# Kernel optimization log

Measured on AMD Instinct MI355X. Metric: run time of the kernel, lower is better.

## Reference

```python
import jax, jax.numpy as jnp
import numpy as np

N, E, G = 8000, 128000, 4
C, NLM, NL = 64, 16, 4
NEL, NB, NH = 10, 8, 64
RMAX = 5.0
PCUT = 5.0
AVG_NEIGH = 16.0
SIGMA = 1.0
LBOX = 6.0
KR = 3
T = 2
LMAP = jnp.array([0, 1, 1, 1, 2, 2, 2, 2, 2, 3, 3, 3, 3, 3, 3, 3])


def _nvec():
    r = np.arange(-KR, KR + 1)
    n = np.stack(np.meshgrid(r, r, r, indexing='ij'), -1).reshape(-1, 3)
    n = n[np.any(n != 0, axis=1)]  # [342,3], k=0 excluded
    return jnp.asarray(n, jnp.float32)


def sph_harm(u):
    # component-normalized real spherical harmonics up to l=3, unit input u [E,3]
    x, y, z = u[:, 0], u[:, 1], u[:, 2]
    one = jnp.ones_like(x)
    c3, c5, c15 = 3.0 ** 0.5, 5.0 ** 0.5, 15.0 ** 0.5
    Y = [one,
         c3 * x, c3 * y, c3 * z,
         c15 * x * y, c15 * y * z, 0.5 * c5 * (3 * z * z - 1.0), c15 * x * z, 0.5 * c15 * (x * x - y * y),
         (35.0 / 8.0) ** 0.5 * y * (3 * x * x - y * y), 105.0 ** 0.5 * x * y * z,
         (21.0 / 8.0) ** 0.5 * y * (5 * z * z - 1.0), 0.5 * 7.0 ** 0.5 * z * (5 * z * z - 3.0),
         (21.0 / 8.0) ** 0.5 * x * (5 * z * z - 1.0), 0.5 * 105.0 ** 0.5 * z * (x * x - y * y),
         (35.0 / 8.0) ** 0.5 * x * (x * x - 3 * y * y)]
    return jnp.stack(Y, -1)  # [E,16]


def radial_basis(r):
    # Bessel basis * polynomial cutoff (MACE RadialEmbeddingBlock)
    u = r / RMAX
    n = jnp.arange(1, NB + 1, dtype=jnp.float32)
    bes = (2.0 / RMAX) ** 0.5 * jnp.sin(n[None, :] * jnp.pi * u[:, None]) / (r[:, None] + 1e-9)
    p = PCUT
    fc = 1.0 - 0.5 * (p + 1) * (p + 2) * u ** p + p * (p + 2) * u ** (p + 1) - 0.5 * p * (p + 1) * u ** (p + 2)
    fc = fc * (u < 1.0)
    return bes * fc[:, None]  # [E,8]


def setup_inputs() -> dict:
    key = jax.random.key(0)
    ks = jax.random.split(key, 24)

    def p(k, shape, fan_in):
        return jax.random.normal(k, shape, jnp.float32) / (fan_in ** 0.5)

    elem = jax.random.randint(ks[0], (N,), 0, NEL)
    inp = {
        'node_attrs': jax.nn.one_hot(elem, NEL, dtype=jnp.float32),
        'positions': jax.random.uniform(ks[1], (N, 3), jnp.float32) * LBOX,
        'shifts': jnp.zeros((E, 3), jnp.float32),
        'density_coefficients': jax.random.normal(ks[2], (N, 1), jnp.float32) * 0.1,
        'cell': jnp.tile(jnp.eye(3, dtype=jnp.float32) * LBOX, (G, 1, 1)),
        'rcell': jnp.tile(jnp.eye(3, dtype=jnp.float32) / LBOX, (G, 1, 1)),
        'volume': jnp.full((G,), LBOX ** 3, jnp.float32),
        'edge_index': jax.random.randint(ks[3], (2, E), 0, N),
        'batch': jnp.repeat(jnp.arange(G), N // G),
        'emb_W': p(ks[4], (NEL, C), NEL),
        'q_coef': p(ks[5], (T, C), 1),
        'rad_W1': p(ks[6], (T, NB, NH), NB),
        'rad_W2': p(ks[7], (T, NH, NH), NH),
        'rad_W3': p(ks[8], (T, NH, NH), NH),
        'rad_W4': p(ks[9], (T, NH, C * NL), NH),
        'lin_up': p(ks[10], (T, NL, C, C), C),
        'lin_out': p(ks[11], (T, NL, C, C), C),
        'W_sc': p(ks[12], (T, NEL, C, C), C),
        'Wp': p(ks[13], (T, 3, C, C), C),
        'W_read0': p(ks[14], (C,), C),
        'Wread1_a': p(ks[15], (C, 16), C),
        'Wread1_b': p(ks[16], (16,), 16),
        'Wq_read': p(ks[17], (T, C), C),
        'atomic_E': jax.random.normal(ks[18], (NEL,), jnp.float32),
    }
    return inp


def reference(node_attrs, positions, shifts, density_coefficients, cell, rcell, volume,
              edge_index, batch, emb_W, q_coef, rad_W1, rad_W2, rad_W3, rad_W4,
              lin_up, lin_out, W_sc, Wp, W_read0, Wread1_a, Wread1_b, Wq_read, atomic_E):
    sender, receiver = edge_index[0], edge_index[1]
    vec = positions[receiver] - positions[sender] + shifts
    r = jnp.linalg.norm(vec, axis=-1)
    Y = sph_harm(vec / (r[:, None] + 1e-9))      # [E,16]
    ef = radial_basis(r)                          # [E,8]

    q = density_coefficients                      # [N,1], max_l=0 multipoles
    feats = jnp.zeros((N, C, NLM), jnp.float32).at[:, :, 0].set(node_attrs @ emb_W)
    e0 = jax.ops.segment_sum(node_attrs @ atomic_E, batch, G)
    energies = [e0]

    for t in range(T):
        # charge-coefficient injection (charge_coefs_linears)
        feats = feats.at[:, :, 0].add(q * q_coef[t][None, :])
        # per-l linear up
        h = jnp.einsum('ncl,lcd->ndl', feats, lin_up[t][LMAP])
        # radial MLP -> per-edge, per-channel, per-l tensor-product weights
        w = jax.nn.silu(ef @ rad_W1[t])
        w = jax.nn.silu(w @ rad_W2[t])
        w = jax.nn.silu(w @ rad_W3[t])
        w = (w @ rad_W4[t]).reshape(E, C, NL)[:, :, LMAP]   # [E,C,16]
        # depthwise equivariant TP message: gather -> contract -> modulate
        hj = h[sender]                                       # [E,C,16]
        s_e = jnp.einsum('ecl,el->ec', hj, Y)                # edge invariant
        m = w * (Y[:, None, :] * s_e[:, :, None])            # [E,C,16]
        A = jax.ops.segment_sum(m, receiver, N) / AVG_NEIGH  # scatter-reduce
        A = jnp.einsum('ncl,lcd->ndl', A, lin_out[t][LMAP])
        # element-dependent residual (self-connection)
        wn = jnp.einsum('nk,kcd->ncd', node_attrs, W_sc[t])
        sc = jnp.einsum('ncd,ncl->ndl', wn, feats)
        # product block: correlation-3 symmetric-contraction surrogate
        s1 = jnp.sum(A * A, axis=2)                           # [N,C]
        out = (jnp.einsum('ncl,cd->ndl', A, Wp[t, 0])
               + jnp.einsum('ncl,cd->ndl', A * s1[:, :, None], Wp[t, 1])
               + jnp.einsum('ncl,cd->ndl', A * (s1 * s1)[:, :, None], Wp[t, 2]))
        feats = out + sc
        # readout
        if t == T - 1:
            node_e = jax.nn.silu(feats[:, :, 0] @ Wread1_a) @ Wread1_b
        else:
            node_e = feats[:, :, 0] @ W_read0
        node_e = node_e + q[:, 0] * (feats[:, :, 0] @ Wq_read[t])
        energies.append(jax.ops.segment_sum(node_e, batch, G))

    # k-space (Ewald-like) electrostatics with Gaussian-smeared charges
    nv = _nvec()                                              # [K,3]
    kvec = 2.0 * jnp.pi * jnp.einsum('kj,gji->gki', nv, rcell)  # [G,K,3]
    k2 = jnp.sum(kvec * kvec, -1)                             # [G,K]
    phase = jnp.einsum('ni,nki->nk', positions, kvec[batch])  # [N,K]
    Sr = jax.ops.segment_sum(q * jnp.cos(phase), batch, G)
    Si = jax.ops.segment_sum(q * jnp.sin(phase), batch, G)
    filt = jnp.exp(-0.5 * SIGMA * SIGMA * k2) / k2
    Ees = (2.0 * jnp.pi / volume) * jnp.sum(filt * (Sr * Sr + Si * Si), axis=1)

    total_energy = jnp.sum(jnp.stack(energies, -1), -1) + Ees
    total_charge = jax.ops.segment_sum(q[:, 0], batch, G)
    dipole = jax.ops.segment_sum(q * positions, batch, G)
    return total_energy, total_charge, dipole
```

## Files before the change

### kernel.cpp

```cpp
#include <hip/hip_runtime.h>
#include <hip/hip_bf16.h>

constexpr int N    = 8000;
constexpr int E    = 128000;
constexpr int G    = 4;
constexpr int NEL  = 10;
constexpr int NGR  = N / G;
constexpr int NC   = N * 64;
constexpr int NK   = 342;
constexpr float RMAX = 5.0f;
constexpr int HS = 72;
constexpr int WS2 = 260;
constexpr int WT_T = 25088;

typedef __bf16 bf16x8 __attribute__((ext_vector_type(8)));
typedef float  f32x4v __attribute__((ext_vector_type(4)));
typedef unsigned short u16x8 __attribute__((ext_vector_type(8)));

__device__ __forceinline__ int lmap_rt(int l) { return (l >= 1) + (l >= 4) + (l >= 9); }
__device__ __forceinline__ float silu(float x) { return x / (1.f + __expf(-x)); }
__device__ __forceinline__ float bf2f(unsigned short u) { return __uint_as_float(((unsigned)u) << 16); }
__device__ __forceinline__ unsigned short f2bf(float f) {
    __hip_bfloat16 h = __float2bfloat16(f);
    return *(unsigned short*)&h;
}

__device__ __forceinline__ void mfma_stage(const unsigned short* hsrc, const unsigned short* wt,
                                           int m0, int lane, f32x4v acc[4], bool k8only)
{
    const int quad = lane >> 4;
    const int idx  = lane & 15;
    bf16x8 bz;
    #pragma unroll
    for (int i = 0; i < 8; ++i) bz[i] = (__bf16)0.f;
    bf16x8 a0 = bz, a1 = bz;
    const int mrow = m0 + idx;
    if (k8only) {
        if (quad == 0) a0 = *(const bf16x8*)&hsrc[mrow * HS];
    } else {
        a0 = *(const bf16x8*)&hsrc[mrow * HS + (quad << 3)];
        a1 = *(const bf16x8*)&hsrc[mrow * HS + 32 + (quad << 3)];
    }
    #pragma unroll
    for (int c4 = 0; c4 < 4; ++c4) {
        const int nrow = (c4 << 4) + idx;
        if (k8only) {
            bf16x8 b0 = bz;
            if (quad == 0) b0 = *(const bf16x8*)&wt[nrow * HS];
            acc[c4] = __builtin_amdgcn_mfma_f32_16x16x32_bf16(a0, b0, acc[c4], 0, 0, 0);
        } else {
            const bf16x8 b0 = *(const bf16x8*)&wt[nrow * HS + (quad << 3)];
            const bf16x8 b1 = *(const bf16x8*)&wt[nrow * HS + 32 + (quad << 3)];
            acc[c4] = __builtin_amdgcn_mfma_f32_16x16x32_bf16(a0, b0, acc[c4], 0, 0, 0);
            acc[c4] = __builtin_amdgcn_mfma_f32_16x16x32_bf16(a1, b1, acc[c4], 0, 0, 0);
        }
    }
}

__global__ __launch_bounds__(256) void k_init(const float* __restrict__ na,
    const float* __restrict__ q, const float* __restrict__ pos,
    const int* __restrict__ batch, const float* __restrict__ aE,
    int* __restrict__ elem, int* __restrict__ counts, float* __restrict__ acc)
{
    __shared__ float s[G * 5];
    if (threadIdx.x < G * 5) s[threadIdx.x] = 0.f;
    __syncthreads();
    const int n = blockIdx.x * 256 + threadIdx.x;
    if (n < N) {
        int el = 0; float best = na[n * NEL];
        #pragma unroll
        for (int j = 1; j < NEL; ++j) { float v = na[n * NEL + j]; if (v > best) { best = v; el = j; } }
        elem[n] = el;
        atomicAdd(&counts[el], 1);
        const int g = batch[n];
        const float qn = q[n];
        atomicAdd(&s[g * 5 + 0], aE[el]);
        atomicAdd(&s[g * 5 + 1], qn);
        atomicAdd(&s[g * 5 + 2], qn * pos[n * 3 + 0]);
        atomicAdd(&s[g * 5 + 3], qn * pos[n * 3 + 1]);
        atomicAdd(&s[g * 5 + 4], qn * pos[n * 3 + 2]);
    }
    __syncthreads();
    if (threadIdx.x < G * 5) atomicAdd(&acc[threadIdx.x], s[threadIdx.x]);
}

__global__ __launch_bounds__(256) void k_feat0(const int* __restrict__ elem,
    const float* __restrict__ embW, float* __restrict__ F)
{
    const int i = blockIdx.x * 256 + threadIdx.x;
    if (i < NC) F[i] = embW[elem[i >> 6] * 64 + (i & 63)];
}

__global__ void k_offs(const int* __restrict__ counts, int* __restrict__ offs)
{
    if (threadIdx.x == 0 && blockIdx.x == 0) {
        int o = 0;
        for (int j = 0; j < NEL; ++j) { offs[j] = o; o += (counts[j] + 63) & ~63; }
        offs[NEL] = o;
    }
}
__global__ __launch_bounds__(256) void k_scatter(const int* __restrict__ elem,
    const int* __restrict__ offs, int* __restrict__ cursor, int* __restrict__ perm)
{
    const int n = blockIdx.x * 256 + threadIdx.x;
    if (n < N) {
        const int el = elem[n];
        const int p = atomicAdd(&cursor[el], 1);
        perm[offs[el] + p] = n;
    }
}

__global__ __launch_bounds__(256) void k_gcnt(const int* __restrict__ ei, int* __restrict__ cnt)
{
    const int e = blockIdx.x * 256 + threadIdx.x;
    if (e < E) atomicAdd(&cnt[ei[E + e]], 1);
}
__global__ __launch_bounds__(1024) void k_goff(const int* __restrict__ cnt, int* __restrict__ roff)
{
    __shared__ int part[1024];
    const int t = threadIdx.x;
    const int base = t * 8;
    int loc[8];
    int s = 0;
    #pragma unroll
    for (int i = 0; i < 8; ++i) { loc[i] = s; s += (base + i < N) ? cnt[base + i] : 0; }
    part[t] = s;
    __syncthreads();
    for (int d = 1; d < 1024; d <<= 1) {
        const int v = (t >= d) ? part[t - d] : 0;
        __syncthreads();
        part[t] += v;
        __syncthreads();
    }
    const int excl = (t == 0) ? 0 : part[t - 1];
    #pragma unroll
    for (int i = 0; i < 8; ++i) if (base + i < N) roff[base + i] = excl + loc[i];
    if (t == 0) roff[N] = E;
}
__global__ __launch_bounds__(256) void k_gscat(const int* __restrict__ ei,
    const int* __restrict__ roff, int* __restrict__ cur, int* __restrict__ elist)
{
    const int e = blockIdx.x * 256 + threadIdx.x;
    if (e < E) {
        const int rv = ei[E + e];
        const int p = atomicAdd(&cur[rv], 1);
        elist[roff[rv] + p] = e;
    }
}

__global__ __launch_bounds__(256) void k_geom(const float* __restrict__ pos,
    const float* __restrict__ shifts, const int* __restrict__ ei,
    const int* __restrict__ elist, float4* __restrict__ geomv, int* __restrict__ spck)
{
    const int j = blockIdx.x * 256 + threadIdx.x;
    if (j >= E) return;
    const int e = elist[j];
    const int s = ei[e], rv = ei[E + e];
    const float dx = pos[rv * 3 + 0] - pos[s * 3 + 0] + shifts[e * 3 + 0];
    const float dy = pos[rv * 3 + 1] - pos[s * 3 + 1] + shifts[e * 3 + 1];
    const float dz = pos[rv * 3 + 2] - pos[s * 3 + 2] + shifts[e * 3 + 2];
    const float r = sqrtf(dx * dx + dy * dy + dz * dz);
    const float inv = 1.f / (r + 1e-9f);
    float4 g;
    g.x = dx * inv; g.y = dy * inv; g.z = dz * inv; g.w = r;
    geomv[j] = g;
    spck[j] = s;
}

__global__ __launch_bounds__(256) void k_wprep_all(const float* __restrict__ rW1,
    const float* __restrict__ rW2, const float* __restrict__ rW3,
    const float* __restrict__ rW4, const float* __restrict__ Wp,
    const float* __restrict__ lup, const float* __restrict__ lout,
    const float* __restrict__ Wsc,
    unsigned short* __restrict__ WT, unsigned short* __restrict__ WpT,
    unsigned short* __restrict__ WlupT, unsigned short* __restrict__ WloutT,
    unsigned short* __restrict__ WscT)
{
    const int gidx = blockIdx.x * 256 + threadIdx.x;
    if (gidx < 2 * WT_T) {
        const int t = gidx / WT_T;
        const int r = gidx % WT_T;
        float v;
        if (r < 512) {
            const int n = r >> 3, k = r & 7;
            v = rW1[t * 512 + k * 64 + n];
        } else if (r < 4608) {
            const int i = r - 512, n = i >> 6, k = i & 63;
            v = rW2[t * 4096 + k * 64 + n];
        } else if (r < 8704) {
            const int i = r - 4608, n = i >> 6, k = i & 63;
            v = rW3[t * 4096 + k * 64 + n];
        } else {
            const int i = r - 8704, n = i >> 6, k = i & 63;
            v = rW4[t * 16384 + k * 256 + n];
        }
        WT[gidx] = f2bf(v);
    } else if (gidx < 2 * WT_T + 24576) {
        const int idx = gidx - 2 * WT_T;
        const int i  = idx & 4095;
        const int d = i >> 6, c = i & 63;
        WpT[idx] = f2bf(Wp[(size_t)(idx >> 12) * 4096 + c * 64 + d]);
    } else if (gidx < 2 * WT_T + 24576 + 32768) {
        const int idx = gidx - (2 * WT_T + 24576);
        const int i = idx & 4095, d = i >> 6, c = i & 63;
        WlupT[idx] = f2bf(lup[(idx >> 12) * 4096 + c * 64 + d]);
    } else if (gidx < 2 * WT_T + 24576 + 65536) {
        const int idx = gidx - (2 * WT_T + 24576 + 32768);
        const int i = idx & 4095, d = i >> 6, c = i & 63;
        WloutT[idx] = f2bf(lout[(idx >> 12) * 4096 + c * 64 + d]);
    } else if (gidx < 2 * WT_T + 24576 + 65536 + 81920) {
        const int idx = gidx - (2 * WT_T + 24576 + 65536);
        const int i = idx & 4095, d = i >> 6, c = i & 63;
        WscT[idx] = f2bf(Wsc[(idx >> 12) * 4096 + c * 64 + d]);
    }
}

__global__ __launch_bounds__(256) void k_lgemm_hb(float* __restrict__ F,
    const float* __restrict__ q, const float* __restrict__ qc,
    const unsigned short* __restrict__ WT, unsigned short* __restrict__ Hb)
{
    __shared__ unsigned short Xb[64 * HS];
    __shared__ unsigned short Wt[64 * HS];
    const int l  = blockIdx.y;
    const int nb = blockIdx.x << 6;
    const int t  = threadIdx.x;
    const int lane = t & 63;
    const int m0   = (t >> 6) << 4;
    const int quad = lane >> 4;
    const int idx  = lane & 15;
    const int prow = t >> 2, pkb = (t & 3) << 4;
    float* Xp = F + (size_t)l * NC + (size_t)nb * 64;
    if (l == 0) {
        #pragma unroll
        for (int k = 0; k < 16; ++k) {
            const int i = t + (k << 8);
            float v = Xp[i] + q[nb + (i >> 6)] * qc[i & 63];
            Xp[i] = v;
            Xb[(i >> 6) * HS + (i & 63)] = f2bf(v);
        }
    } else {
        #pragma unroll
        for (int k = 0; k < 16; ++k) {
            const int i = t + (k << 8);
            Xb[(i >> 6) * HS + (i & 63)] = f2bf(Xp[i]);
        }
    }
    const unsigned short* W = WT + lmap_rt(l) * 4096;
    *(u16x8*)&Wt[prow * HS + pkb]     = *(const u16x8*)&W[prow * 64 + pkb];
    *(u16x8*)&Wt[prow * HS + pkb + 8] = *(const u16x8*)&W[prow * 64 + pkb + 8];
    __syncthreads();
    f32x4v acc[4];
    #pragma unroll
    for (int c = 0; c < 4; ++c) { acc[c][0] = 0.f; acc[c][1] = 0.f; acc[c][2] = 0.f; acc[c][3] = 0.f; }
    mfma_stage(Xb, Wt, m0, lane, acc, false);
    #pragma unroll
    for (int c4 = 0; c4 < 4; ++c4) {
        #pragma unroll
        for (int r = 0; r < 4; ++r) {
            const int n = nb + m0 + (quad << 2) + r;
            const int col = (c4 << 4) + idx;
            Hb[(size_t)n * 1024 + (l << 6) + col] = f2bf(acc[c4][r]);
        }
    }
}

__global__ __launch_bounds__(256) void k_hbT(const unsigned short* __restrict__ Hb,
    unsigned short* __restrict__ HbT)
{
    const int n = (blockIdx.x << 2) + (threadIdx.x >> 6);
    const int c = threadIdx.x & 63;
    u16x8 a, b;
    #pragma unroll
    for (int l = 0; l < 8; ++l) {
        a[l] = Hb[(size_t)n * 1024 + (l << 6) + c];
        b[l] = Hb[(size_t)n * 1024 + ((l + 8) << 6) + c];
    }
    *(u16x8*)&HbT[(size_t)n * 1024 + c * 16]     = a;
    *(u16x8*)&HbT[(size_t)n * 1024 + c * 16 + 8] = b;
}

__global__ __launch_bounds__(256) void k_lgemm(const float* __restrict__ X,
    const unsigned short* __restrict__ WT, float* __restrict__ Out)
{
    __shared__ unsigned short Xb[64 * HS];
    __shared__ unsigned short Wt[64 * HS];
    const int l  = blockIdx.y;
    const int nb = blockIdx.x << 6;
    const int t  = threadIdx.x;
    const int lane = t & 63;
    const int m0   = (t >> 6) << 4;
    const int quad = lane >> 4;
    const int idx  = lane & 15;
    const int prow = t >> 2, pkb = (t & 3) << 4;
    const float* Xp = X + (size_t)l * NC + (size_t)nb * 64;
    #pragma unroll
    for (int k = 0; k < 16; ++k) {
        const int i = t + (k << 8);
        Xb[(i >> 6) * HS + (i & 63)] = f2bf(Xp[i]);
    }
    const unsigned short* W = WT + lmap_rt(l) * 4096;
    *(u16x8*)&Wt[prow * HS + pkb]     = *(const u16x8*)&W[prow * 64 + pkb];
    *(u16x8*)&Wt[prow * HS + pkb + 8] = *(const u16x8*)&W[prow * 64 + pkb + 8];
    __syncthreads();
    f32x4v acc[4];
    #pragma unroll
    for (int c = 0; c < 4; ++c) { acc[c][0] = 0.f; acc[c][1] = 0.f; acc[c][2] = 0.f; acc[c][3] = 0.f; }
    mfma_stage(Xb, Wt, m0, lane, acc, false);
    float* Op = Out + (size_t)l * NC + (size_t)nb * 64;
    #pragma unroll
    for (int c4 = 0; c4 < 4; ++c4) {
        #pragma unroll
        for (int r = 0; r < 4; ++r) {
            const int row = m0 + (quad << 2) + r;
            Op[(row << 6) + (c4 << 4) + idx] = acc[c4][r];
        }
    }
}

__global__ __launch_bounds__(256) void k_sc(const float* __restrict__ F,
    const unsigned short* __restrict__ WscT, const int* __restrict__ perm,
    const int* __restrict__ elem, float* __restrict__ Out)
{
    __shared__ unsigned short Xb[64 * HS];
    __shared__ unsigned short Wt[64 * HS];
    __shared__ int rows[64];
    const int l  = blockIdx.y;
    const int tb = blockIdx.x << 6;
    const int t  = threadIdx.x;
    if (t < 64) rows[t] = perm[tb + t];
    __syncthreads();
    if (rows[0] < 0) return;
    const int lane = t & 63;
    const int m0   = (t >> 6) << 4;
    const int quad = lane >> 4;
    const int idx  = lane & 15;
    const int prow = t >> 2, pkb = (t & 3) << 4;
    const unsigned short* W = WscT + elem[rows[0]] * 4096;
    *(u16x8*)&Wt[prow * HS + pkb]     = *(const u16x8*)&W[prow * 64 + pkb];
    *(u16x8*)&Wt[prow * HS + pkb + 8] = *(const u16x8*)&W[prow * 64 + pkb + 8];
    #pragma unroll
    for (int k = 0; k < 16; ++k) {
        const int i = t + (k << 8);
        const int rr = i >> 6, cc = i & 63;
        const int n = rows[rr];
        Xb[rr * HS + cc] = (n >= 0) ? f2bf(F[(size_t)l * NC + (size_t)n * 64 + cc]) : (unsigned short)0;
    }
    __syncthreads();
    f32x4v acc[4];
    #pragma unroll
    for (int c = 0; c < 4; ++c) { acc[c][0] = 0.f; acc[c][1] = 0.f; acc[c][2] = 0.f; acc[c][3] = 0.f; }
    mfma_stage(Xb, Wt, m0, lane, acc, false);
    #pragma unroll
    for (int c4 = 0; c4 < 4; ++c4) {
        #pragma unroll
        for (int r = 0; r < 4; ++r) {
            const int n = rows[m0 + (quad << 2) + r];
            if (n >= 0) Out[(size_t)l * NC + (size_t)n * 64 + (c4 << 4) + idx] = acc[c4][r];
        }
    }
}

__global__ __launch_bounds__(256) void k_edge(const float4* __restrict__ geomv,
    const int* __restrict__ spck, const unsigned short* __restrict__ WT,
    const unsigned short* __restrict__ HbT, const int* __restrict__ roff,
    float* __restrict__ A)
{
    __shared__ unsigned short hbf[64 * HS];
    __shared__ unsigned short wtb[64 * HS];
    __shared__ unsigned short wfull[64 * WS2];
    __shared__ float geos[64 * 4];
    __shared__ int   sps[64];
    __shared__ int   rinfo[2];
    const int t = threadIdx.x;
    const int lane = t & 63;
    const int wid  = t >> 6;
    const int m0   = wid << 4;
    const int quad = lane >> 4;
    const int idx  = lane & 15;
    const int prow = t >> 2, pkb = (t & 3) << 4;
    const int w0 = blockIdx.x << 6;
    const int w1 = w0 + 64;
    if (t == 0) {
        int lo = 0, hi = N - 1;
        while (lo < hi) { const int mid = (lo + hi + 1) >> 1; if (roff[mid] <= w0) lo = mid; else hi = mid - 1; }
        rinfo[0] = lo;
    } else if (t == 1) {
        const int w1m = w0 + 63;
        int lo = 0, hi = N - 1;
        while (lo < hi) { const int mid = (lo + hi + 1) >> 1; if (roff[mid] <= w1m) lo = mid; else hi = mid - 1; }
        rinfo[1] = lo;
    }
    if (t < 64) {
        const float4 g = geomv[w0 + t];
        *(float4*)&geos[t * 4] = g;
        sps[t] = spck[w0 + t];
        const float r = g.w;
        const float u  = r * 0.2f;
        const float u2 = u * u, u5 = u2 * u2 * u;
        const float fc = 1.f - 21.f * u5 + 35.f * u5 * u - 15.f * u5 * u2;
        float pref = 0.63245553f * fc / (r + 1e-9f);
        if (u >= 1.f) pref = 0.f;
        const float piu = 3.14159265358979f * u;
        #pragma unroll
        for (int b = 0; b < 8; ++b) hbf[t * HS + b] = f2bf(__sinf((float)(b + 1) * piu) * pref);
    }
    {
        const int n = t >> 2, k = (t & 3) << 1;
        wtb[n * HS + k]     = WT[n * 8 + k];
        wtb[n * HS + k + 1] = WT[n * 8 + k + 1];
    }
    u16x8 pf0 = *(const u16x8*)&WT[512 + prow * 64 + pkb];
    u16x8 pf1 = *(const u16x8*)&WT[512 + prow * 64 + pkb + 8];
    __syncthreads();
    f32x4v acc[4];
    #pragma unroll
    for (int c = 0; c < 4; ++c) { acc[c][0] = 0.f; acc[c][1] = 0.f; acc[c][2] = 0.f; acc[c][3] = 0.f; }
    mfma_stage(hbf, wtb, m0, lane, acc, true);
    __syncthreads();
    #pragma unroll
    for (int c4 = 0; c4 < 4; ++c4)
        #pragma unroll
        for (int r = 0; r < 4; ++r)
            hbf[(m0 + (quad << 2) + r) * HS + (c4 << 4) + idx] = f2bf(silu(acc[c4][r]));
    *(u16x8*)&wtb[prow * HS + pkb]     = pf0;
    *(u16x8*)&wtb[prow * HS + pkb + 8] = pf1;
    pf0 = *(const u16x8*)&WT[4608 + prow * 64 + pkb];
    pf1 = *(const u16x8*)&WT[4608 + prow * 64 + pkb + 8];
    __syncthreads();
    #pragma unroll
    for (int c = 0; c < 4; ++c) { acc[c][0] = 0.f; acc[c][1] = 0.f; acc[c][2] = 0.f; acc[c][3] = 0.f; }
    mfma_stage(hbf, wtb, m0, lane, acc, false);
    __syncthreads();
    #pragma unroll
    for (int c4 = 0; c4 < 4; ++c4)
        #pragma unroll
        for (int r = 0; r < 4; ++r)
            hbf[(m0 + (quad << 2) + r) * HS + (c4 << 4) + idx] = f2bf(silu(acc[c4][r]));
    *(u16x8*)&wtb[prow * HS + pkb]     = pf0;
    *(u16x8*)&wtb[prow * HS + pkb + 8] = pf1;
    pf0 = *(const u16x8*)&WT[8704 + prow * 64 + pkb];
    pf1 = *(const u16x8*)&WT[8704 + prow * 64 + pkb + 8];
    __syncthreads();
    #pragma unroll
    for (int c = 0; c < 4; ++c) { acc[c][0] = 0.f; acc[c][1] = 0.f; acc[c][2] = 0.f; acc[c][3] = 0.f; }
    mfma_stage(hbf, wtb, m0, lane, acc, false);
    __syncthreads();
    #pragma unroll
    for (int c4 = 0; c4 < 4; ++c4)
        #pragma unroll
        for (int r = 0; r < 4; ++r)
            hbf[(m0 + (quad << 2) + r) * HS + (c4 << 4) + idx] = f2bf(silu(acc[c4][r]));
    *(u16x8*)&wtb[prow * HS + pkb]     = pf0;
    *(u16x8*)&wtb[prow * HS + pkb + 8] = pf1;
    pf0 = *(const u16x8*)&WT[8704 + 4096 + prow * 64 + pkb];
    pf1 = *(const u16x8*)&WT[8704 + 4096 + prow * 64 + pkb + 8];
    __syncthreads();
    for (int cc = 0; cc < 4; ++cc) {
        #pragma unroll
        for (int c = 0; c < 4; ++c) { acc[c][0] = 0.f; acc[c][1] = 0.f; acc[c][2] = 0.f; acc[c][3] = 0.f; }
        mfma_stage(hbf, wtb, m0, lane, acc, false);
        __syncthreads();
        #pragma unroll
        for (int c4 = 0; c4 < 4; ++c4)
            #pragma unroll
            for (int r = 0; r < 4; ++r)
                wfull[(m0 + (quad << 2) + r) * WS2 + (cc << 6) + (c4 << 4) + idx] = f2bf(acc[c4][r]);
        if (cc < 3) {
            *(u16x8*)&wtb[prow * HS + pkb]     = pf0;
            *(u16x8*)&wtb[prow * HS + pkb + 8] = pf1;
            if (cc < 2) {
                pf0 = *(const u16x8*)&WT[8704 + (cc + 2) * 4096 + prow * 64 + pkb];
                pf1 = *(const u16x8*)&WT[8704 + (cc + 2) * 4096 + prow * 64 + pkb + 8];
            }
        }
        __syncthreads();
    }
    const int r0 = rinfo[0], r1 = rinfo[1];
    constexpr int LM[16] = {0,1,1,1,2,2,2,2,2,3,3,3,3,3,3,3};
    for (int r = r0 + wid; r <= r1; r += 4) {
        const int ra = roff[r], rb = roff[r + 1];
        const int ja = ra > w0 ? ra : w0;
        const int jb = rb < w1 ? rb : w1;
        float a16[16];
        #pragma unroll
        for (int l = 0; l < 16; ++l) a16[l] = 0.f;
        if (ja < jb) {
            u16x8 hA0, hB0, hA1, hB1;
            {
                const int s = sps[ja - w0];
                hA0 = *(const u16x8*)&HbT[(size_t)s * 1024 + lane * 16];
                hB0 = *(const u16x8*)&HbT[(size_t)s * 1024 + lane * 16 + 8];
            }
            hA1 = hA0; hB1 = hB0;
            if (ja + 1 < jb) {
                const int s = sps[ja + 1 - w0];
                hA1 = *(const u16x8*)&HbT[(size_t)s * 1024 + lane * 16];
                hB1 = *(const u16x8*)&HbT[(size_t)s * 1024 + lane * 16 + 8];
            }
            for (int j = ja; j < jb; ++j) {
                const int jj = j - w0;
                float hc[16];
                #pragma unroll
                for (int l = 0; l < 8; ++l) { hc[l] = bf2f(hA0[l]); hc[l + 8] = bf2f(hB0[l]); }
                hA0 = hA1; hB0 = hB1;
                if (j + 2 < jb) {
                    const int s = sps[jj + 2];
                    hA1 = *(const u16x8*)&HbT[(size_t)s * 1024 + lane * 16];
                    hB1 = *(const u16x8*)&HbT[(size_t)s * 1024 + lane * 16 + 8];
                }
                const float gr = geos[jj * 4 + 3];
                if (gr >= RMAX) continue;
                const float x = geos[jj * 4], y = geos[jj * 4 + 1], z = geos[jj * 4 + 2];
                const float xx = x * x, yy = y * y, zz = z * z;
                float Y[16];
                Y[0] = 1.f;
                Y[1] = 1.7320508f * x;  Y[2] = 1.7320508f * y;  Y[3] = 1.7320508f * z;
                Y[4] = 3.8729833f * x * y;  Y[5] = 3.8729833f * y * z;
                Y[6] = 0.5f * 2.2360680f * (3.f * zz - 1.f);
                Y[7] = 3.8729833f * x * z;  Y[8] = 0.5f * 3.8729833f * (xx - yy);
                Y[9]  = 2.0916500f * y * (3.f * xx - yy);
                Y[10] = 10.2469508f * x * y * z;
                Y[11] = 1.6201852f * y * (5.f * zz - 1.f);
                Y[12] = 0.5f * 2.6457513f * z * (5.f * zz - 3.f);
                Y[13] = 1.6201852f * x * (5.f * zz - 1.f);
                Y[14] = 0.5f * 10.2469508f * z * (xx - yy);
                Y[15] = 2.0916500f * x * (xx - 3.f * yy);
                float se = 0.f;
                #pragma unroll
                for (int l = 0; l < 16; ++l) se += hc[l] * Y[l];
                se *= 0.0625f;
                const ushort4 wq = *(const ushort4*)&wfull[jj * WS2 + (lane << 2)];
                const float wl[4] = { bf2f(wq.x) * se, bf2f(wq.y) * se, bf2f(wq.z) * se, bf2f(wq.w) * se };
                #pragma unroll
                for (int l = 0; l < 16; ++l) a16[l] += wl[LM[l]] * Y[l];
            }
        }
        float* Ap = A + (size_t)r * 64 + lane;
        if (ra >= w0 && rb <= w1) {
            #pragma unroll
            for (int l = 0; l < 16; ++l) Ap[(size_t)l * NC] = a16[l];
        } else {
            #pragma unroll
            for (int l = 0; l < 16; ++l) atomicAdd(&Ap[(size_t)l * NC], a16[l]);
        }
    }
}

__global__ __launch_bounds__(256) void k_s1(const float* __restrict__ H, float* __restrict__ s1)
{
    const int i = blockIdx.x * 256 + threadIdx.x;
    if (i < NC) {
        float s = 0.f;
        #pragma unroll
        for (int l = 0; l < 16; ++l) { const float a = H[(size_t)l * NC + i]; s += a * a; }
        s1[i] = s;
    }
}

__global__ __launch_bounds__(256) void k_out(const float* __restrict__ Ap,
    const float* __restrict__ s1, const unsigned short* __restrict__ WpT,
    const float* __restrict__ sc, float* __restrict__ F)
{
    __shared__ unsigned short Xb[64 * HS];
    __shared__ unsigned short Wt[64 * HS];
    const int l  = blockIdx.y;
    const int nb = blockIdx.x << 6;
    const int t  = threadIdx.x;
    const int lane = t & 63;
    const int m0   = (t >> 6) << 4;
    const int quad = lane >> 4;
    const int idx  = lane & 15;
    const int prow = t >> 2, pkb = (t & 3) << 4;
    const float* Xp = Ap + (size_t)l * NC + (size_t)nb * 64;
    float av[16], sv[16];
    #pragma unroll
    for (int k = 0; k < 16; ++k) {
        const int i = t + (k << 8);
        av[k] = Xp[i];
        sv[k] = s1[nb * 64 + i];
    }
    f32x4v acc[4];
    #pragma unroll
    for (int c = 0; c < 4; ++c) { acc[c][0] = 0.f; acc[c][1] = 0.f; acc[c][2] = 0.f; acc[c][3] = 0.f; }
    for (int p = 0; p < 3; ++p) {
        #pragma unroll
        for (int k = 0; k < 16; ++k) {
            const int i = t + (k << 8);
            Xb[(i >> 6) * HS + (i & 63)] = f2bf(av[k]);
            av[k] *= sv[k];
        }
        *(u16x8*)&Wt[prow * HS + pkb]     = *(const u16x8*)&WpT[p * 4096 + prow * 64 + pkb];
        *(u16x8*)&Wt[prow * HS + pkb + 8] = *(const u16x8*)&WpT[p * 4096 + prow * 64 + pkb + 8];
        __syncthreads();
        mfma_stage(Xb, Wt, m0, lane, acc, false);
        __syncthreads();
    }
    #pragma unroll
    for (int c4 = 0; c4 < 4; ++c4) {
        #pragma unroll
        for (int r = 0; r < 4; ++r) {
            const int row = m0 + (quad << 2) + r;
            const int col = (c4 << 4) + idx;
            const size_t id = (size_t)l * NC + (size_t)(nb + row) * 64 + col;
            F[id] = acc[c4][r] + sc[id];
        }
    }
}

__global__ __launch_bounds__(256) void k_read(const float* __restrict__ F,
    const float* __restrict__ q, const int* __restrict__ batch,
    const float* __restrict__ Wr0, const float* __restrict__ Wa,
    const float* __restrict__ Wb, const float* __restrict__ Wq,
    float* __restrict__ acc, int last)
{
    __shared__ float sred[G];
    if (threadIdx.x < G) sred[threadIdx.x] = 0.f;
    __syncthreads();
    const int n = blockIdx.x * 256 + threadIdx.x;
    if (n < N) {
        float a16[16];
        #pragma unroll
        for (int j = 0; j < 16; ++j) a16[j] = 0.f;
        float ar = 0.f, aq = 0.f;
        const float* f = F + (size_t)n * 64;
        for (int c = 0; c < 64; ++c) {
            const float fv = f[c];
            aq += fv * Wq[c];
            if (last) {
                #pragma unroll
                for (int j = 0; j < 16; ++j) a16[j] += fv * Wa[c * 16 + j];
            } else ar += fv * Wr0[c];
        }
        float en;
        if (last) {
            en = 0.f;
            #pragma unroll
            for (int j = 0; j < 16; ++j) en += silu(a16[j]) * Wb[j];
        } else en = ar;
        en += q[n] * aq;
        atomicAdd(&sred[batch[n]], en);
    }
    __syncthreads();
    if (threadIdx.x < G) atomicAdd(&acc[threadIdx.x * 5], sred[threadIdx.x]);
}

__global__ __launch_bounds__(256) void k_kvec(const float* __restrict__ rcell,
    float* __restrict__ kvec, float* __restrict__ k2)
{
    const int idx = blockIdx.x * 256 + threadIdx.x;
    if (idx >= G * NK) return;
    const int g = idx / NK, k = idx % NK;
    const int kk = k + (k >= 171 ? 1 : 0);
    const int a = kk / 49 - 3, b = (kk / 7) % 7 - 3, c = kk % 7 - 3;
    const float* rc = rcell + g * 9;
    float s = 0.f;
    #pragma unroll
    for (int i = 0; i < 3; ++i) {
        const float kv = 6.283185307f * ((float)a * rc[0 + i] + (float)b * rc[3 + i] + (float)c * rc[6 + i]);
        kvec[idx * 3 + i] = kv;
        s += kv * kv;
    }
    k2[idx] = s;
}

__global__ __launch_bounds__(256) void k_phase(const float* __restrict__ pos,
    const float* __restrict__ q, const float* __restrict__ kvec,
    float* __restrict__ Sr, float* __restrict__ Si)
{
    __shared__ float kvs[38 * 3];
    __shared__ float srs[38], sis[38];
    const int g = blockIdx.z, kc = blockIdx.x, ncb = blockIdx.y;
    const int kbase = kc * 38;
    if (threadIdx.x < 38 * 3) kvs[threadIdx.x] = kvec[((size_t)g * NK + kbase) * 3 + threadIdx.x];
    if (threadIdx.x < 38) { srs[threadIdx.x] = 0.f; sis[threadIdx.x] = 0.f; }
    __syncthreads();
    const int t = threadIdx.x;
    float px = 0.f, py = 0.f, pz = 0.f, qn = 0.f;
    if (t < 250) {
        const int n = g * NGR + ncb * 250 + t;
        px = pos[n * 3]; py = pos[n * 3 + 1]; pz = pos[n * 3 + 2]; qn = q[n];
    }
    const int lane = t & 63;
    for (int j = 0; j < 38; ++j) {
        const float ph = px * kvs[j * 3] + py * kvs[j * 3 + 1] + pz * kvs[j * 3 + 2];
        float sv, cv;
        __sincosf(ph, &sv, &cv);
        float vr = qn * cv, vi = qn * sv;
        #pragma unroll
        for (int o = 32; o > 0; o >>= 1) { vr += __shfl_down(vr, o, 64); vi += __shfl_down(vi, o, 64); }
        if (lane == 0) { atomicAdd(&srs[j], vr); atomicAdd(&sis[j], vi); }
    }
    __syncthreads();
    if (t < 38) {
        atomicAdd(&Sr[g * NK + kbase + t], srs[t]);
        atomicAdd(&Si[g * NK + kbase + t], sis[t]);
    }
}

__global__ __launch_bounds__(512) void k_final(const float* __restrict__ k2,
    const float* __restrict__ Sr, const float* __restrict__ Si,
    const float* __restrict__ vol, const float* __restrict__ acc,
    float* __restrict__ out)
{
    __shared__ float red[512];
    const int g = blockIdx.x, t = threadIdx.x;
    float v = 0.f;
    if (t < NK) {
        const float kk = k2[g * NK + t];
        const float sr = Sr[g * NK + t], si = Si[g * NK + t];
        v = __expf(-0.5f * kk) * (sr * sr + si * si) / kk;
    }
    red[t] = v;
    __syncthreads();
    for (int s2 = 256; s2 > 0; s2 >>= 1) {
        if (t < s2) red[t] += red[t + s2];
        __syncthreads();
    }
    if (t == 0) {
        const float Ees = 6.283185307f / vol[g] * red[0];
        out[g]     = acc[g * 5 + 0] + Ees;
        out[4 + g] = acc[g * 5 + 1];
        out[8 + g * 3 + 0] = acc[g * 5 + 2];
        out[8 + g * 3 + 1] = acc[g * 5 + 3];
        out[8 + g * 3 + 2] = acc[g * 5 + 4];
    }
}

extern "C" void kernel_launch(void* const* d_in, const int* in_sizes, int n_in,
                              void* d_out, int out_size, void* d_ws, size_t ws_size,
                              hipStream_t stream)
{
    const float* na    = (const float*)d_in[0];
    const float* pos   = (const float*)d_in[1];
    const float* shif  = (const float*)d_in[2];
    const float* q     = (const float*)d_in[3];
    const float* rcell = (const float*)d_in[5];
    const float* vol   = (const float*)d_in[6];
    const int*   ei    = (const int*)d_in[7];
    const int*   batch = (const int*)d_in[8];
    const float* embW  = (const float*)d_in[9];
    const float* qcoef = (const float*)d_in[10];
    const float* rW1   = (const float*)d_in[11];
    const float* rW2   = (const float*)d_in[12];
    const float* rW3   = (const float*)d_in[13];
    const float* rW4   = (const float*)d_in[14];
    const float* lup   = (const float*)d_in[15];
    const float* lout  = (const float*)d_in[16];
    const float* Wsc   = (const float*)d_in[17];
    const float* Wp    = (const float*)d_in[18];
    const float* Wr0   = (const float*)d_in[19];
    const float* Wa    = (const float*)d_in[20];
    const float* Wb    = (const float*)d_in[21];
    const float* Wq    = (const float*)d_in[22];
    const float* aE    = (const float*)d_in[23];
    float* out = (float*)d_out;

    float* wsf  = (float*)d_ws;
    float* F    = wsf;
    float* A    = F + 8192000;
    float* R    = A + 8192000;
    float* H2   = R;
    unsigned short* HbT   = (unsigned short*)R;
    unsigned short* Hbtmp = (unsigned short*)(R + 4096000);
    float* s1   = R + 20480000;
    float* kvec = s1 + 512000;
    float* k2   = kvec + 4104;
    float* Sr   = k2 + 1368;
    float* Si   = Sr + 1368;
    float* acc  = Si + 1368;
    int*   elem = (int*)(acc + 32);
    int*   perm = elem + 8000;
    int*   counts = perm + 8640;
    int*   cursor = counts + 16;
    int*   offs   = cursor + 16;
    int*   roff   = offs + 16;
    int*   cnt    = roff + 8001;
    int*   cur    = cnt + 8000;
    int*   elist  = cur + 8000;
    unsigned short* WTb = (unsigned short*)(((uintptr_t)(elist + E) + 31) & ~(uintptr_t)31);
    unsigned short* WpT = WTb + 2 * WT_T;
    float4* geomv = (float4*)(WpT + 24576);
    int*    spck  = (int*)(geomv + E);
    unsigned short* WlupT  = (unsigned short*)(spck + E);
    unsigned short* WloutT = WlupT + 32768;
    unsigned short* WscT   = WloutT + 32768;

    hipMemsetAsync(F, 0, 8192000 * sizeof(float), stream);
    hipMemsetAsync(Sr, 0, (1368 * 2 + 32) * sizeof(float), stream);
    hipMemsetAsync(perm, 0xFF, 8640 * sizeof(int), stream);
    hipMemsetAsync(counts, 0, 32 * sizeof(int), stream);
    hipMemsetAsync(cnt, 0, 16000 * sizeof(int), stream);

    k_init<<<32, 256, 0, stream>>>(na, q, pos, batch, aE, elem, counts, acc);
    k_feat0<<<2000, 256, 0, stream>>>(elem, embW, F);
    k_offs<<<1, 64, 0, stream>>>(counts, offs);
    k_scatter<<<32, 256, 0, stream>>>(elem, offs, cursor, perm);
    k_gcnt<<<500, 256, 0, stream>>>(ei, cnt);
    k_goff<<<1, 1024, 0, stream>>>(cnt, roff);
    k_gscat<<<500, 256, 0, stream>>>(ei, roff, cur, elist);
    k_geom<<<500, 256, 0, stream>>>(pos, shif, ei, elist, geomv, spck);
    k_wprep_all<<<868, 256, 0, stream>>>(rW1, rW2, rW3, rW4, Wp, lup, lout, Wsc,
                                         WTb, WpT, WlupT, WloutT, WscT);
    k_kvec<<<6, 256, 0, stream>>>(rcell, kvec, k2);
    k_phase<<<dim3(9, 8, G), 256, 0, stream>>>(pos, q, kvec, Sr, Si);

    for (int t = 0; t < 2; ++t) {
        k_lgemm_hb<<<dim3(125, 16), 256, 0, stream>>>(F, q, qcoef + t * 64, WlupT + t * 16384, Hbtmp);
        k_hbT<<<2000, 256, 0, stream>>>(Hbtmp, HbT);
        hipMemsetAsync(A, 0, 8192000 * sizeof(float), stream);
        k_edge<<<2000, 256, 0, stream>>>(geomv, spck, WTb + t * WT_T, HbT, roff, A);
        k_lgemm<<<dim3(125, 16), 256, 0, stream>>>(A, WloutT + t * 16384, H2);
        k_s1<<<2000, 256, 0, stream>>>(H2, s1);
        k_sc<<<dim3(135, 16), 256, 0, stream>>>(F, WscT + t * 40960, perm, elem, A);
        k_out<<<dim3(125, 16), 256, 0, stream>>>(H2, s1, WpT + t * 12288, A, F);
        k_read<<<32, 256, 0, stream>>>(F, q, batch, Wr0, Wa, Wb, Wq + t * 64, acc, t == 1);
    }
    k_final<<<G, 512, 0, stream>>>(k2, Sr, Si, vol, acc, out);
}
```

Before: 564.3 us.

## Store node features, H2 and self-connection buffers in bf16 with vectorized loads

Node feature tensor F, the linear-out result H2 and the self-connection output are now stored as bf16 instead of fp32. This halves the memory traffic across several per-layer kernels (lgemm_hb, lgemm, s1, sc, out, read), and those kernels switch to 16-byte vector loads and stores. The cost is extra rounding of the residual stream and intermediates to bf16, which can accumulate error across interactions.

```diff
diff --git a/kernel.cpp b/kernel.cpp
--- a/kernel.cpp
+++ b/kernel.cpp
@@ -85,10 +85,10 @@
 }
 
 __global__ __launch_bounds__(256) void k_feat0(const int* __restrict__ elem,
-    const float* __restrict__ embW, float* __restrict__ F)
+    const float* __restrict__ embW, unsigned short* __restrict__ Fb)
 {
     const int i = blockIdx.x * 256 + threadIdx.x;
-    if (i < NC) F[i] = embW[elem[i >> 6] * 64 + (i & 63)];
+    if (i < NC) Fb[i] = f2bf(embW[elem[i >> 6] * 64 + (i & 63)]);
 }
 
 __global__ void k_offs(const int* __restrict__ counts, int* __restrict__ offs)
@@ -215,7 +215,7 @@
     }
 }
 
-__global__ __launch_bounds__(256) void k_lgemm_hb(float* __restrict__ F,
+__global__ __launch_bounds__(256) void k_lgemm_hb(unsigned short* __restrict__ Fb,
     const float* __restrict__ q, const float* __restrict__ qc,
     const unsigned short* __restrict__ WT, unsigned short* __restrict__ Hb)
 {
@@ -229,21 +229,23 @@
     const int quad = lane >> 4;
     const int idx  = lane & 15;
     const int prow = t >> 2, pkb = (t & 3) << 4;
-    float* Xp = F + (size_t)l * NC + (size_t)nb * 64;
+    unsigned short* Xp = Fb + (size_t)l * NC + (size_t)nb * 64;
     if (l == 0) {
-        #pragma unroll
-        for (int k = 0; k < 16; ++k) {
-            const int i = t + (k << 8);
-            float v = Xp[i] + q[nb + (i >> 6)] * qc[i & 63];
-            Xp[i] = v;
-            Xb[(i >> 6) * HS + (i & 63)] = f2bf(v);
-        }
+        const float qn = q[nb + prow];
+        u16x8 x0 = *(const u16x8*)&Xp[prow * 64 + pkb];
+        u16x8 x1 = *(const u16x8*)&Xp[prow * 64 + pkb + 8];
+        #pragma unroll
+        for (int j = 0; j < 8; ++j) {
+            x0[j] = f2bf(bf2f(x0[j]) + qn * qc[pkb + j]);
+            x1[j] = f2bf(bf2f(x1[j]) + qn * qc[pkb + 8 + j]);
+        }
+        *(u16x8*)&Xp[prow * 64 + pkb]     = x0;
+        *(u16x8*)&Xp[prow * 64 + pkb + 8] = x1;
+        *(u16x8*)&Xb[prow * HS + pkb]     = x0;
+        *(u16x8*)&Xb[prow * HS + pkb + 8] = x1;
     } else {
-        #pragma unroll
-        for (int k = 0; k < 16; ++k) {
-            const int i = t + (k << 8);
-            Xb[(i >> 6) * HS + (i & 63)] = f2bf(Xp[i]);
-        }
+        *(u16x8*)&Xb[prow * HS + pkb]     = *(const u16x8*)&Xp[prow * 64 + pkb];
+        *(u16x8*)&Xb[prow * HS + pkb + 8] = *(const u16x8*)&Xp[prow * 64 + pkb + 8];
     }
     const unsigned short* W = WT + lmap_rt(l) * 4096;
     *(u16x8*)&Wt[prow * HS + pkb]     = *(const u16x8*)&W[prow * 64 + pkb];
@@ -280,7 +282,7 @@
 }
 
 __global__ __launch_bounds__(256) void k_lgemm(const float* __restrict__ X,
-    const unsigned short* __restrict__ WT, float* __restrict__ Out)
+    const unsigned short* __restrict__ WT, unsigned short* __restrict__ H2b)
 {
     __shared__ unsigned short Xb[64 * HS];
     __shared__ unsigned short Wt[64 * HS];
@@ -306,20 +308,20 @@
     #pragma unroll
     for (int c = 0; c < 4; ++c) { acc[c][0] = 0.f; acc[c][1] = 0.f; acc[c][2] = 0.f; acc[c][3] = 0.f; }
     mfma_stage(Xb, Wt, m0, lane, acc, false);
-    float* Op = Out + (size_t)l * NC + (size_t)nb * 64;
+    unsigned short* Op = H2b + (size_t)l * NC + (size_t)nb * 64;
     #pragma unroll
     for (int c4 = 0; c4 < 4; ++c4) {
         #pragma unroll
         for (int r = 0; r < 4; ++r) {
             const int row = m0 + (quad << 2) + r;
-            Op[(row << 6) + (c4 << 4) + idx] = acc[c4][r];
-        }
-    }
-}
-
-__global__ __launch_bounds__(256) void k_sc(const float* __restrict__ F,
+            Op[(row << 6) + (c4 << 4) + idx] = f2bf(acc[c4][r]);
+        }
+    }
+}
+
+__global__ __launch_bounds__(256) void k_sc(const unsigned short* __restrict__ Fb,
     const unsigned short* __restrict__ WscT, const int* __restrict__ perm,
-    const int* __restrict__ elem, float* __restrict__ Out)
+    const int* __restrict__ elem, unsigned short* __restrict__ scb)
 {
     __shared__ unsigned short Xb[64 * HS];
     __shared__ unsigned short Wt[64 * HS];
@@ -338,12 +340,19 @@
     const unsigned short* W = WscT + elem[rows[0]] * 4096;
     *(u16x8*)&Wt[prow * HS + pkb]     = *(const u16x8*)&W[prow * 64 + pkb];
     *(u16x8*)&Wt[prow * HS + pkb + 8] = *(const u16x8*)&W[prow * 64 + pkb + 8];
-    #pragma unroll
-    for (int k = 0; k < 16; ++k) {
-        const int i = t + (k << 8);
-        const int rr = i >> 6, cc = i & 63;
-        const int n = rows[rr];
-        Xb[rr * HS + cc] = (n >= 0) ? f2bf(F[(size_t)l * NC + (size_t)n * 64 + cc]) : (unsigned short)0;
+    {
+        const int n = rows[prow];
+        u16x8 z;
+        #pragma unroll
+        for (int j = 0; j < 8; ++j) z[j] = 0;
+        u16x8 x0 = z, x1 = z;
+        if (n >= 0) {
+            const unsigned short* src = Fb + (size_t)l * NC + (size_t)n * 64 + pkb;
+            x0 = *(const u16x8*)&src[0];
+            x1 = *(const u16x8*)&src[8];
+        }
+        *(u16x8*)&Xb[prow * HS + pkb]     = x0;
+        *(u16x8*)&Xb[prow * HS + pkb + 8] = x1;
     }
     __syncthreads();
     f32x4v acc[4];
@@ -355,7 +364,7 @@
         #pragma unroll
         for (int r = 0; r < 4; ++r) {
             const int n = rows[m0 + (quad << 2) + r];
-            if (n >= 0) Out[(size_t)l * NC + (size_t)n * 64 + (c4 << 4) + idx] = acc[c4][r];
+            if (n >= 0) scb[(size_t)l * NC + (size_t)n * 64 + (c4 << 4) + idx] = f2bf(acc[c4][r]);
         }
     }
 }
@@ -546,20 +555,20 @@
     }
 }
 
-__global__ __launch_bounds__(256) void k_s1(const float* __restrict__ H, float* __restrict__ s1)
+__global__ __launch_bounds__(256) void k_s1(const unsigned short* __restrict__ H2b, float* __restrict__ s1)
 {
     const int i = blockIdx.x * 256 + threadIdx.x;
     if (i < NC) {
         float s = 0.f;
         #pragma unroll
-        for (int l = 0; l < 16; ++l) { const float a = H[(size_t)l * NC + i]; s += a * a; }
+        for (int l = 0; l < 16; ++l) { const float a = bf2f(H2b[(size_t)l * NC + i]); s += a * a; }
         s1[i] = s;
     }
 }
 
-__global__ __launch_bounds__(256) void k_out(const float* __restrict__ Ap,
+__global__ __launch_bounds__(256) void k_out(const unsigned short* __restrict__ H2b,
     const float* __restrict__ s1, const unsigned short* __restrict__ WpT,
-    const float* __restrict__ sc, float* __restrict__ F)
+    const unsigned short* __restrict__ scb, unsigned short* __restrict__ Fb)
 {
     __shared__ unsigned short Xb[64 * HS];
     __shared__ unsigned short Wt[64 * HS];
@@ -571,24 +580,30 @@
     const int quad = lane >> 4;
     const int idx  = lane & 15;
     const int prow = t >> 2, pkb = (t & 3) << 4;
-    const float* Xp = Ap + (size_t)l * NC + (size_t)nb * 64;
+    const unsigned short* Xp = H2b + (size_t)l * NC + (size_t)nb * 64;
     float av[16], sv[16];
-    #pragma unroll
-    for (int k = 0; k < 16; ++k) {
-        const int i = t + (k << 8);
-        av[k] = Xp[i];
-        sv[k] = s1[nb * 64 + i];
+    {
+        const u16x8 x0 = *(const u16x8*)&Xp[prow * 64 + pkb];
+        const u16x8 x1 = *(const u16x8*)&Xp[prow * 64 + pkb + 8];
+        #pragma unroll
+        for (int j = 0; j < 8; ++j) { av[j] = bf2f(x0[j]); av[8 + j] = bf2f(x1[j]); }
+        #pragma unroll
+        for (int j = 0; j < 4; ++j) {
+            const float4 s4 = *(const float4*)&s1[(nb + prow) * 64 + pkb + (j << 2)];
+            sv[j * 4] = s4.x; sv[j * 4 + 1] = s4.y; sv[j * 4 + 2] = s4.z; sv[j * 4 + 3] = s4.w;
+        }
     }
     f32x4v acc[4];
     #pragma unroll
     for (int c = 0; c < 4; ++c) { acc[c][0] = 0.f; acc[c][1] = 0.f; acc[c][2] = 0.f; acc[c][3] = 0.f; }
     for (int p = 0; p < 3; ++p) {
-        #pragma unroll
-        for (int k = 0; k < 16; ++k) {
-            const int i = t + (k << 8);
-            Xb[(i >> 6) * HS + (i & 63)] = f2bf(av[k]);
-            av[k] *= sv[k];
-        }
+        u16x8 x0, x1;
+        #pragma unroll
+        for (int j = 0; j < 8; ++j) { x0[j] = f2bf(av[j]); x1[j] = f2bf(av[8 + j]); }
+        *(u16x8*)&Xb[prow * HS + pkb]     = x0;
+        *(u16x8*)&Xb[prow * HS + pkb + 8] = x1;
+        #pragma unroll
+        for (int k = 0; k < 16; ++k) av[k] *= sv[k];
         *(u16x8*)&Wt[prow * HS + pkb]     = *(const u16x8*)&WpT[p * 4096 + prow * 64 + pkb];
         *(u16x8*)&Wt[prow * HS + pkb + 8] = *(const u16x8*)&WpT[p * 4096 + prow * 64 + pkb + 8];
         __syncthreads();
@@ -602,12 +617,12 @@
             const int row = m0 + (quad << 2) + r;
             const int col = (c4 << 4) + idx;
             const size_t id = (size_t)l * NC + (size_t)(nb + row) * 64 + col;
-            F[id] = acc[c4][r] + sc[id];
-        }
-    }
-}
-
-__global__ __launch_bounds__(256) void k_read(const float* __restrict__ F,
+            Fb[id] = f2bf(acc[c4][r] + bf2f(scb[id]));
+        }
+    }
+}
+
+__global__ __launch_bounds__(256) void k_read(const unsigned short* __restrict__ Fb,
     const float* __restrict__ q, const int* __restrict__ batch,
     const float* __restrict__ Wr0, const float* __restrict__ Wa,
     const float* __restrict__ Wb, const float* __restrict__ Wq,
@@ -622,9 +637,9 @@
         #pragma unroll
         for (int j = 0; j < 16; ++j) a16[j] = 0.f;
         float ar = 0.f, aq = 0.f;
-        const float* f = F + (size_t)n * 64;
+        const unsigned short* f = Fb + (size_t)n * 64;
         for (int c = 0; c < 64; ++c) {
-            const float fv = f[c];
+            const float fv = bf2f(f[c]);
             aq += fv * Wq[c];
             if (last) {
                 #pragma unroll
@@ -756,10 +771,11 @@
     float* out = (float*)d_out;
 
     float* wsf  = (float*)d_ws;
-    float* F    = wsf;
-    float* A    = F + 8192000;
+    unsigned short* Fb = (unsigned short*)wsf;
+    float* A    = wsf + 8192000;
+    unsigned short* scb = (unsigned short*)A;
     float* R    = A + 8192000;
-    float* H2   = R;
+    unsigned short* H2b   = (unsigned short*)R;
     unsigned short* HbT   = (unsigned short*)R;
     unsigned short* Hbtmp = (unsigned short*)(R + 4096000);
     float* s1   = R + 20480000;
@@ -785,14 +801,14 @@
     unsigned short* WloutT = WlupT + 32768;
     unsigned short* WscT   = WloutT + 32768;
 
-    hipMemsetAsync(F, 0, 8192000 * sizeof(float), stream);
+    hipMemsetAsync(Fb, 0, 8192000 * sizeof(unsigned short), stream);
     hipMemsetAsync(Sr, 0, (1368 * 2 + 32) * sizeof(float), stream);
     hipMemsetAsync(perm, 0xFF, 8640 * sizeof(int), stream);
     hipMemsetAsync(counts, 0, 32 * sizeof(int), stream);
     hipMemsetAsync(cnt, 0, 16000 * sizeof(int), stream);
 
     k_init<<<32, 256, 0, stream>>>(na, q, pos, batch, aE, elem, counts, acc);
-    k_feat0<<<2000, 256, 0, stream>>>(elem, embW, F);
+    k_feat0<<<2000, 256, 0, stream>>>(elem, embW, Fb);
     k_offs<<<1, 64, 0, stream>>>(counts, offs);
     k_scatter<<<32, 256, 0, stream>>>(elem, offs, cursor, perm);
     k_gcnt<<<500, 256, 0, stream>>>(ei, cnt);
@@ -805,15 +821,15 @@
     k_phase<<<dim3(9, 8, G), 256, 0, stream>>>(pos, q, kvec, Sr, Si);
 
     for (int t = 0; t < 2; ++t) {
-        k_lgemm_hb<<<dim3(125, 16), 256, 0, stream>>>(F, q, qcoef + t * 64, WlupT + t * 16384, Hbtmp);
+        k_lgemm_hb<<<dim3(125, 16), 256, 0, stream>>>(Fb, q, qcoef + t * 64, WlupT + t * 16384, Hbtmp);
         k_hbT<<<2000, 256, 0, stream>>>(Hbtmp, HbT);
         hipMemsetAsync(A, 0, 8192000 * sizeof(float), stream);
         k_edge<<<2000, 256, 0, stream>>>(geomv, spck, WTb + t * WT_T, HbT, roff, A);
-        k_lgemm<<<dim3(125, 16), 256, 0, stream>>>(A, WloutT + t * 16384, H2);
-        k_s1<<<2000, 256, 0, stream>>>(H2, s1);
-        k_sc<<<dim3(135, 16), 256, 0, stream>>>(F, WscT + t * 40960, perm, elem, A);
-        k_out<<<dim3(125, 16), 256, 0, stream>>>(H2, s1, WpT + t * 12288, A, F);
-        k_read<<<32, 256, 0, stream>>>(F, q, batch, Wr0, Wa, Wb, Wq + t * 64, acc, t == 1);
+        k_lgemm<<<dim3(125, 16), 256, 0, stream>>>(A, WloutT + t * 16384, H2b);
+        k_s1<<<2000, 256, 0, stream>>>(H2b, s1);
+        k_sc<<<dim3(135, 16), 256, 0, stream>>>(Fb, WscT + t * 40960, perm, elem, scb);
+        k_out<<<dim3(125, 16), 256, 0, stream>>>(H2b, s1, WpT + t * 12288, scb, Fb);
+        k_read<<<32, 256, 0, stream>>>(Fb, q, batch, Wr0, Wa, Wb, Wq + t * 64, acc, t == 1);
     }
     k_final<<<G, 512, 0, stream>>>(k2, Sr, Si, vol, acc, out);
 }
```

Result: faster. 533.2 us (-5.5%).
